# Kernel tuning notes

Measured on AMD Instinct MI355X. Metric: run time of the kernel, lower is better.

## Reference

```python
import jax, jax.numpy as jnp
import numpy as np

ALPHA = 0.1          # LeakyReLU negative slope
NEG = -9.0e15        # mask fill value (matches torch source)
S_OUT = 64           # source_out_features
T_OUT = 64           # target_out_features


def setup_inputs() -> dict:
    key = jax.random.key(0)
    ks = jax.random.split(key, 8)
    n_s, n_t = 8192, 4096
    s_in, t_in = 128, 128
    hs = jax.random.normal(ks[0], (n_s, s_in), dtype=jnp.float32)
    ht = jax.random.normal(ks[1], (n_t, t_in), dtype=jnp.float32)
    A_opt = jax.random.randint(ks[2], (n_t, n_s), 0, 2, dtype=jnp.int32)
    # xavier_uniform with gain=1.414
    def xavier(k, shape, gain=1.414):
        fan_in, fan_out = shape[0], shape[1]
        bound = gain * np.sqrt(6.0 / (fan_in + fan_out))
        return jax.random.uniform(k, shape, jnp.float32, -bound, bound)
    Ws = xavier(ks[3], (s_in, T_OUT))
    Wt = xavier(ks[4], (t_in, S_OUT))
    a1 = xavier(ks[5], (S_OUT + T_OUT, 1))
    bias_s = jnp.zeros((T_OUT,), jnp.float32)
    bias_t = jnp.zeros((S_OUT,), jnp.float32)
    return {"hs": hs, "ht": ht, "A_opt": A_opt, "Ws": Ws, "Wt": Wt,
            "a1": a1, "bias_s": bias_s, "bias_t": bias_t}


def reference(hs, ht, A_opt, Ws, Wt, a1, bias_s, bias_t):
    # Asymmetric HOAN, eval mode (dropout=0), concatenate=True.
    Whs = hs @ Ws                       # [n_s, t_out]
    Wht = ht @ Wt                       # [n_t, s_out]
    # a1 split: first S_OUT rows pair with Wht, remaining T_OUT rows with Whs
    a_t = a1[:S_OUT, :]                 # [s_out, 1]
    a_s = a1[S_OUT:, :]                 # [t_out, 1]
    Whst = Whs @ a_s                    # [n_s, 1]
    Whtt = Wht @ a_t                    # [n_t, 1]
    e_st = jax.nn.leaky_relu(Whtt + Whst.T, ALPHA)   # [n_t, n_s]
    e_ts = jax.nn.leaky_relu(Whst + Whtt.T, ALPHA)   # [n_s, n_t]
    mask = A_opt > 0                    # [n_t, n_s]
    att_st = jax.nn.softmax(jnp.where(mask, e_st, NEG), axis=1)
    h_prime_st = att_st @ Whs + bias_s  # [n_t, t_out]
    att_ts = jax.nn.softmax(jnp.where(mask.T, e_ts, NEG), axis=1)
    h_prime_ts = att_ts @ Wht + bias_t  # [n_s, s_out]
    return jax.nn.elu(h_prime_st), jax.nn.elu(h_prime_ts)
```

## Files before the change

kernel.cpp:

```cpp
#include <hip/hip_runtime.h>
#include <math.h>

#define N_S 8192
#define N_T 4096
#define DIN 128
#define NF  64
#define SPL0 8
#define SPL1 8

typedef __attribute__((ext_vector_type(8))) short short8;
typedef __attribute__((ext_vector_type(4))) float f32x4;
typedef unsigned long long u64;
typedef unsigned int u32;

__device__ __forceinline__ unsigned short f2bf(float x){
  unsigned u = __float_as_uint(x);
  unsigned r = (u + 0x7fffu + ((u >> 16) & 1u)) >> 16;
  return (unsigned short)r;
}

__device__ __forceinline__ size_t xt2_idx(int f, int k){
  return ((size_t)(k >> 5))*2048 + (size_t)((f >> 4)*512 + ((k >> 3) & 3)*128 + (f & 15)*8 + (k & 7));
}

__global__ __launch_bounds__(256) void k1_fused(
    const int* __restrict__ A,
    u64* __restrict__ RBt,
    u64* __restrict__ CBt,
    const float* __restrict__ hs, const float* __restrict__ ht,
    const float* __restrict__ Ws, const float* __restrict__ Wt,
    const float* __restrict__ a1,
    unsigned short* __restrict__ XT2s, unsigned short* __restrict__ XT2t,
    float* __restrict__ Es, float* __restrict__ Fs,
    float* __restrict__ Et, float* __restrict__ Ft)
{
  __shared__ __align__(16) float smem[DIN*NF + 4*DIN];
  int bx = blockIdx.x;
  int t = threadIdx.x;
  if (bx < 2048) {
    unsigned* T4 = (unsigned*)smem;
    int i0 = (bx & 63) * 64;
    int j0 = (bx >> 6) * 256;
    int w = t >> 6, l = t & 63;
    int4 v[16];
    #pragma unroll
    for (int it = 0; it < 16; ++it)
      v[it] = *(const int4*)&A[(size_t)(i0 + w*16 + it)*N_S + j0 + 4*l];
    #pragma unroll
    for (int rg = 0; rg < 4; ++rg) {
      unsigned p = 0;
      #pragma unroll
      for (int rr = 0; rr < 4; ++rr) {
        int4 m = v[rg*4 + rr];
        unsigned nib = (m.x > 0 ? 1u : 0u) | (m.y > 0 ? 2u : 0u)
                     | (m.z > 0 ? 4u : 0u) | (m.w > 0 ? 8u : 0u);
        p |= nib << (8*rr);
      }
      T4[(w*4 + rg)*65 + l] = p;
    }
    __syncthreads();
    {
      int r = t & 63, g = t >> 6;
      u64 bits = 0;
      #pragma unroll
      for (int i = 0; i < 16; ++i) {
        unsigned word = T4[(r >> 2)*65 + g*16 + i];
        unsigned nib = (word >> (8*(r & 3))) & 0xFu;
        bits |= (u64)nib << (4*i);
      }
      RBt[(size_t)((j0 >> 6) + g)*N_T + i0 + r] = bits;
    }
    {
      int c = t;
      u64 bits = 0;
      #pragma unroll
      for (int rg = 0; rg < 16; ++rg) {
        unsigned word = T4[rg*65 + (c >> 2)];
        unsigned x = (word >> (c & 3)) & 0x01010101u;
        unsigned nib = (x * 0x01020408u) >> 24;
        bits |= (u64)(nib & 0xFu) << (4*rg);
      }
      CBt[(size_t)(i0 >> 6)*N_S + j0 + c] = bits;
    }
  } else {
    int b = bx - 2048;
    float* Wl = smem;
    float* hrow = smem + DIN*NF;
    bool is_s = b < (N_S/4);
    const float* h; const float* W; const float* av;
    unsigned short* XT; float* Ed; float* Fd; int r0;
    if (is_s) { r0 = b*4;           h = hs; W = Ws; av = a1 + 64; XT = XT2s; Ed = Es; Fd = Fs; }
    else      { r0 = (b - N_S/4)*4; h = ht; W = Wt; av = a1;      XT = XT2t; Ed = Et; Fd = Ft; }
    for (int i = t; i < DIN*NF; i += 256) Wl[i] = W[i];
    for (int i = t; i < 4*DIN;  i += 256) hrow[i] = h[(size_t)r0*DIN + i];
    __syncthreads();
    int f = t & 63, sr = t >> 6;
    float acc = 0.f;
    #pragma unroll 8
    for (int k = 0; k < DIN; ++k) acc += hrow[sr*DIN + k] * Wl[k*NF + f];
    int r = r0 + sr;
    XT[xt2_idx(f, r)] = f2bf(acc);
    float p = acc * av[f];
    #pragma unroll
    for (int o = 32; o > 0; o >>= 1) p += __shfl_xor(p, o, 64);
    if (f == 0) { Ed[r] = __expf(p); Fd[r] = __expf(0.1f*p); }
  }
}

template<int DIR>
__device__ __forceinline__ void agg_body(
    int rb, int split,
    const u64* __restrict__ MBt,
    const float* __restrict__ EuT, const float* __restrict__ FuT,
    const float* __restrict__ EkT, const float* __restrict__ FkT,
    const unsigned short* __restrict__ XT2,
    float* __restrict__ accP,
    float* __restrict__ sumP)
{
  constexpr int NK = (DIR == 0) ? N_S : N_T;
  constexpr int NU = (DIR == 0) ? N_T : N_S;
  constexpr int SPL = (DIR == 0) ? SPL0 : SPL1;
  constexpr int KCH = NK / SPL;
  int t = threadIdx.x;
  int wave = t >> 6, l = t & 63;
  int row16 = l & 15, grp = l >> 4;
  int u = rb*64 + wave*16 + row16;
  float Eu = EuT[u], Fu = FuT[u];
  f32x4 acc[4];
  #pragma unroll
  for (int q = 0; q < 4; ++q) { acc[q][0]=0.f; acc[q][1]=0.f; acc[q][2]=0.f; acc[q][3]=0.f; }
  f32x4 accs; accs[0]=0.f; accs[1]=0.f; accs[2]=0.f; accs[3]=0.f;
  short8 bones;
  #pragma unroll
  for (int j = 0; j < 8; ++j) bones[j] = (short)0x3F80;
  int kc0 = split * KCH;

  #pragma unroll 2
  for (int k0 = kc0; k0 < kc0 + KCH; k0 += 64) {
    u64 mb = MBt[(size_t)(k0 >> 6)*NU + u];
    u32 mlo = (u32)mb, mhi = (u32)(mb >> 32);
    short8 af01[2];
    #pragma unroll
    for (int h = 0; h < 2; ++h) {
      int kb = k0 + 32*h + grp*8;
      float4 e0 = *(const float4*)&EkT[kb];
      float4 e1 = *(const float4*)&EkT[kb + 4];
      float4 f0 = *(const float4*)&FkT[kb];
      float4 f1 = *(const float4*)&FkT[kb + 4];
      float w0 = fmaxf(Eu*e0.x, Fu*f0.x);
      float w1 = fmaxf(Eu*e0.y, Fu*f0.y);
      float w2 = fmaxf(Eu*e0.z, Fu*f0.z);
      float w3 = fmaxf(Eu*e0.w, Fu*f0.w);
      float w4 = fmaxf(Eu*e1.x, Fu*f1.x);
      float w5 = fmaxf(Eu*e1.y, Fu*f1.y);
      float w6 = fmaxf(Eu*e1.z, Fu*f1.z);
      float w7 = fmaxf(Eu*e1.w, Fu*f1.w);
      u32 bb = ((h ? mhi : mlo) >> (grp*8)) & 0xffu;
      float wv[8] = {w0,w1,w2,w3,w4,w5,w6,w7};
      union { u32 uu[4]; short8 v; } pk;
      #pragma unroll
      for (int p = 0; p < 4; ++p) {
        int j = 2*p;
        int slo = ((int)(bb << (31 - j))) >> 31;
        int shi = ((int)(bb << (30 - j))) >> 31;
        u32 msk = __builtin_amdgcn_perm((u32)shi, (u32)slo, 0x05040100u);
        u32 w01 = __builtin_amdgcn_perm(__float_as_uint(wv[j+1]),
                                        __float_as_uint(wv[j]), 0x07060302u);
        pk.uu[p] = w01 & msk;
      }
      af01[h] = pk.v;
    }
    const unsigned short* xb = XT2 + ((size_t)(k0 >> 5))*2048 + l*8;
    #pragma unroll
    for (int q = 0; q < 4; ++q) {
      short8 b0 = *(const short8*)(xb + q*512);
      short8 b1 = *(const short8*)(xb + 2048 + q*512);
      acc[q] = __builtin_amdgcn_mfma_f32_16x16x32_bf16(af01[0], b0, acc[q], 0, 0, 0);
      acc[q] = __builtin_amdgcn_mfma_f32_16x16x32_bf16(af01[1], b1, acc[q], 0, 0, 0);
    }
    accs = __builtin_amdgcn_mfma_f32_16x16x32_bf16(af01[0], bones, accs, 0, 0, 0);
    accs = __builtin_amdgcn_mfma_f32_16x16x32_bf16(af01[1], bones, accs, 0, 0, 0);
  }

  if (row16 == 0) {
    #pragma unroll
    for (int r = 0; r < 4; ++r)
      sumP[(size_t)split*NU + rb*64 + wave*16 + grp*4 + r] = accs[r];
  }
  float* ap = accP + (size_t)split*NU*NF;
  #pragma unroll
  for (int q = 0; q < 4; ++q) {
    #pragma unroll
    for (int r = 0; r < 4; ++r) {
      int uo = rb*64 + wave*16 + grp*4 + r;
      ap[(size_t)uo*NF + q*16 + row16] = acc[q][r];
    }
  }
}

__global__ __launch_bounds__(256, 8) void agg_fused(
    const u64* __restrict__ RBt, const u64* __restrict__ CBt,
    const float* __restrict__ Es, const float* __restrict__ Fs,
    const float* __restrict__ Et, const float* __restrict__ Ft,
    const unsigned short* __restrict__ XT2s, const unsigned short* __restrict__ XT2t,
    float* __restrict__ P0, float* __restrict__ S0,
    float* __restrict__ P1, float* __restrict__ S1)
{
  int b = blockIdx.x;
  if (b < 64*SPL0) {
    agg_body<0>(b & 63, b >> 6, RBt, Et, Ft, Es, Fs, XT2s, P0, S0);
  } else {
    int b2 = b - 64*SPL0;
    agg_body<1>(b2 & 127, b2 >> 7, CBt, Es, Fs, Et, Ft, XT2t, P1, S1);
  }
}

__global__ __launch_bounds__(256) void finalize_kernel(
    const float* __restrict__ P0, const float* __restrict__ S0,
    const float* __restrict__ P1, const float* __restrict__ S1,
    const float* __restrict__ bias_s, const float* __restrict__ bias_t,
    float* __restrict__ out)
{
  int tid = blockIdx.x*256 + threadIdx.x;
  const int n0 = N_T*NF/4;
  float4 a = make_float4(0.f, 0.f, 0.f, 0.f);
  float den = 0.f;
  float4 bias;
  if (tid < n0) {
    int u = tid >> 4, fq = (tid & 15)*4;
    #pragma unroll
    for (int s = 0; s < SPL0; ++s) {
      float4 p = *(const float4*)&P0[((size_t)s*N_T + u)*NF + fq];
      a.x += p.x; a.y += p.y; a.z += p.z; a.w += p.w;
      den += S0[(size_t)s*N_T + u];
    }
    bias = *(const float4*)&bias_s[fq];
  } else {
    int i2 = tid - n0;
    int u = i2 >> 4, fq = (i2 & 15)*4;
    #pragma unroll
    for (int s = 0; s < SPL1; ++s) {
      float4 p = *(const float4*)&P1[((size_t)s*N_S + u)*NF + fq];
      a.x += p.x; a.y += p.y; a.z += p.z; a.w += p.w;
      den += S1[(size_t)s*N_S + u];
    }
    bias = *(const float4*)&bias_t[fq];
  }
  float inv = den > 0.f ? 1.f/den : 0.f;
  float4 v;
  v.x = a.x*inv + bias.x; v.y = a.y*inv + bias.y;
  v.z = a.z*inv + bias.z; v.w = a.w*inv + bias.w;
  v.x = v.x > 0.f ? v.x : expm1f(v.x);
  v.y = v.y > 0.f ? v.y : expm1f(v.y);
  v.z = v.z > 0.f ? v.z : expm1f(v.z);
  v.w = v.w > 0.f ? v.w : expm1f(v.w);
  *(float4*)&out[tid*4] = v;
}

extern "C" void kernel_launch(void* const* d_in, const int* in_sizes, int n_in,
                              void* d_out, int out_size, void* d_ws, size_t ws_size,
                              hipStream_t stream)
{
  const float* hs     = (const float*)d_in[0];
  const float* ht     = (const float*)d_in[1];
  const int*   A      = (const int*)  d_in[2];
  const float* Ws     = (const float*)d_in[3];
  const float* Wt     = (const float*)d_in[4];
  const float* a1     = (const float*)d_in[5];
  const float* bias_s = (const float*)d_in[6];
  const float* bias_t = (const float*)d_in[7];
  float* out = (float*)d_out;

  u64* RBt = (u64*)d_ws;
  u64* CBt = RBt + (size_t)(N_S/64)*N_T;
  unsigned short* XT2s = (unsigned short*)(CBt + (size_t)(N_T/64)*N_S);
  unsigned short* XT2t = XT2s + (size_t)NF*N_S;
  float* Es = (float*)(XT2t + (size_t)NF*N_T);
  float* Fs = Es + N_S;
  float* Et = Fs + N_S;
  float* Ft = Et + N_T;
  float* P0 = Ft + N_T;
  float* S0 = P0 + (size_t)SPL0*N_T*NF;
  float* P1 = S0 + (size_t)SPL0*N_T;
  float* S1 = P1 + (size_t)SPL1*N_S*NF;

  k1_fused<<<2048 + (N_S + N_T)/4, 256, 0, stream>>>(A, RBt, CBt, hs, ht, Ws, Wt, a1,
                                                     XT2s, XT2t, Es, Fs, Et, Ft);
  agg_fused<<<64*SPL0 + 128*SPL1, 256, 0, stream>>>(RBt, CBt, Es, Fs, Et, Ft,
                                                    XT2s, XT2t, P0, S0, P1, S1);
  finalize_kernel<<<(N_T*NF + N_S*NF)/1024, 256, 0, stream>>>(P0, S0, P1, S1,
                                                              bias_s, bias_t, out);
}
```

Before: 89.58 us.

## Interleave E/F arrays, chunk W staging, nontemporal mask loads, fewer splits

Stores the E and F exponentials for each node interleaved in one array, so the aggregation loop reads one stream of contiguous float4 pairs instead of two separate arrays. The projection blocks now stage W in 16-row chunks, cutting shared memory from about 33KB to about 6KB to raise occupancy, at the cost of extra barriers. The mask-packing loads of A use nontemporal hints to avoid polluting cache. The reverse-direction split count drops from 8 to 4, which means fewer partial sums to reduce but also fewer blocks in flight.

```diff
diff --git a/kernel.cpp b/kernel.cpp
--- a/kernel.cpp
+++ b/kernel.cpp
@@ -6,10 +6,11 @@
 #define DIN 128
 #define NF  64
 #define SPL0 8
-#define SPL1 8
+#define SPL1 4
 
 typedef __attribute__((ext_vector_type(8))) short short8;
 typedef __attribute__((ext_vector_type(4))) float f32x4;
+typedef __attribute__((ext_vector_type(4))) int i32x4;
 typedef unsigned long long u64;
 typedef unsigned int u32;
 
@@ -31,10 +32,9 @@
     const float* __restrict__ Ws, const float* __restrict__ Wt,
     const float* __restrict__ a1,
     unsigned short* __restrict__ XT2s, unsigned short* __restrict__ XT2t,
-    float* __restrict__ Es, float* __restrict__ Fs,
-    float* __restrict__ Et, float* __restrict__ Ft)
-{
-  __shared__ __align__(16) float smem[DIN*NF + 4*DIN];
+    float* __restrict__ EFs, float* __restrict__ EFt)
+{
+  __shared__ __align__(16) float smem[16*64 + 4*DIN];
   int bx = blockIdx.x;
   int t = threadIdx.x;
   if (bx < 2048) {
@@ -42,16 +42,17 @@
     int i0 = (bx & 63) * 64;
     int j0 = (bx >> 6) * 256;
     int w = t >> 6, l = t & 63;
-    int4 v[16];
+    i32x4 v[16];
     #pragma unroll
     for (int it = 0; it < 16; ++it)
-      v[it] = *(const int4*)&A[(size_t)(i0 + w*16 + it)*N_S + j0 + 4*l];
+      v[it] = __builtin_nontemporal_load(
+          (const i32x4*)&A[(size_t)(i0 + w*16 + it)*N_S + j0 + 4*l]);
     #pragma unroll
     for (int rg = 0; rg < 4; ++rg) {
       unsigned p = 0;
       #pragma unroll
       for (int rr = 0; rr < 4; ++rr) {
-        int4 m = v[rg*4 + rr];
+        i32x4 m = v[rg*4 + rr];
         unsigned nib = (m.x > 0 ? 1u : 0u) | (m.y > 0 ? 2u : 0u)
                      | (m.z > 0 ? 4u : 0u) | (m.w > 0 ? 8u : 0u);
         p |= nib << (8*rr);
@@ -85,25 +86,30 @@
   } else {
     int b = bx - 2048;
     float* Wl = smem;
-    float* hrow = smem + DIN*NF;
+    float* hrow = smem + 16*64;
     bool is_s = b < (N_S/4);
     const float* h; const float* W; const float* av;
-    unsigned short* XT; float* Ed; float* Fd; int r0;
-    if (is_s) { r0 = b*4;           h = hs; W = Ws; av = a1 + 64; XT = XT2s; Ed = Es; Fd = Fs; }
-    else      { r0 = (b - N_S/4)*4; h = ht; W = Wt; av = a1;      XT = XT2t; Ed = Et; Fd = Ft; }
-    for (int i = t; i < DIN*NF; i += 256) Wl[i] = W[i];
-    for (int i = t; i < 4*DIN;  i += 256) hrow[i] = h[(size_t)r0*DIN + i];
-    __syncthreads();
+    unsigned short* XT; float* EFd; int r0;
+    if (is_s) { r0 = b*4;           h = hs; W = Ws; av = a1 + 64; XT = XT2s; EFd = EFs; }
+    else      { r0 = (b - N_S/4)*4; h = ht; W = Wt; av = a1;      XT = XT2t; EFd = EFt; }
+    for (int i = t; i < 4*DIN; i += 256) hrow[i] = h[(size_t)r0*DIN + i];
     int f = t & 63, sr = t >> 6;
     float acc = 0.f;
-    #pragma unroll 8
-    for (int k = 0; k < DIN; ++k) acc += hrow[sr*DIN + k] * Wl[k*NF + f];
+    #pragma unroll
+    for (int c = 0; c < 8; ++c) {
+      __syncthreads();
+      #pragma unroll
+      for (int i = t; i < 16*64; i += 256) Wl[i] = W[(c*16 + (i >> 6))*NF + (i & 63)];
+      __syncthreads();
+      #pragma unroll
+      for (int kk = 0; kk < 16; ++kk) acc += hrow[sr*DIN + c*16 + kk] * Wl[kk*64 + f];
+    }
     int r = r0 + sr;
     XT[xt2_idx(f, r)] = f2bf(acc);
     float p = acc * av[f];
     #pragma unroll
     for (int o = 32; o > 0; o >>= 1) p += __shfl_xor(p, o, 64);
-    if (f == 0) { Ed[r] = __expf(p); Fd[r] = __expf(0.1f*p); }
+    if (f == 0) { EFd[2*r] = __expf(p); EFd[2*r + 1] = __expf(0.1f*p); }
   }
 }
 
@@ -111,8 +117,7 @@
 __device__ __forceinline__ void agg_body(
     int rb, int split,
     const u64* __restrict__ MBt,
-    const float* __restrict__ EuT, const float* __restrict__ FuT,
-    const float* __restrict__ EkT, const float* __restrict__ FkT,
+    const float* __restrict__ EFu, const float* __restrict__ EFk,
     const unsigned short* __restrict__ XT2,
     float* __restrict__ accP,
     float* __restrict__ sumP)
@@ -125,7 +130,8 @@
   int wave = t >> 6, l = t & 63;
   int row16 = l & 15, grp = l >> 4;
   int u = rb*64 + wave*16 + row16;
-  float Eu = EuT[u], Fu = FuT[u];
+  float2 ef = *(const float2*)&EFu[2*u];
+  float Eu = ef.x, Fu = ef.y;
   f32x4 acc[4];
   #pragma unroll
   for (int q = 0; q < 4; ++q) { acc[q][0]=0.f; acc[q][1]=0.f; acc[q][2]=0.f; acc[q][3]=0.f; }
@@ -143,20 +149,16 @@
     #pragma unroll
     for (int h = 0; h < 2; ++h) {
       int kb = k0 + 32*h + grp*8;
-      float4 e0 = *(const float4*)&EkT[kb];
-      float4 e1 = *(const float4*)&EkT[kb + 4];
-      float4 f0 = *(const float4*)&FkT[kb];
-      float4 f1 = *(const float4*)&FkT[kb + 4];
-      float w0 = fmaxf(Eu*e0.x, Fu*f0.x);
-      float w1 = fmaxf(Eu*e0.y, Fu*f0.y);
-      float w2 = fmaxf(Eu*e0.z, Fu*f0.z);
-      float w3 = fmaxf(Eu*e0.w, Fu*f0.w);
-      float w4 = fmaxf(Eu*e1.x, Fu*f1.x);
-      float w5 = fmaxf(Eu*e1.y, Fu*f1.y);
-      float w6 = fmaxf(Eu*e1.z, Fu*f1.z);
-      float w7 = fmaxf(Eu*e1.w, Fu*f1.w);
+      float4 p0 = *(const float4*)&EFk[2*kb];
+      float4 p1 = *(const float4*)&EFk[2*kb + 4];
+      float4 p2 = *(const float4*)&EFk[2*kb + 8];
+      float4 p3 = *(const float4*)&EFk[2*kb + 12];
+      float wv[8];
+      wv[0] = fmaxf(Eu*p0.x, Fu*p0.y); wv[1] = fmaxf(Eu*p0.z, Fu*p0.w);
+      wv[2] = fmaxf(Eu*p1.x, Fu*p1.y); wv[3] = fmaxf(Eu*p1.z, Fu*p1.w);
+      wv[4] = fmaxf(Eu*p2.x, Fu*p2.y); wv[5] = fmaxf(Eu*p2.z, Fu*p2.w);
+      wv[6] = fmaxf(Eu*p3.x, Fu*p3.y); wv[7] = fmaxf(Eu*p3.z, Fu*p3.w);
       u32 bb = ((h ? mhi : mlo) >> (grp*8)) & 0xffu;
-      float wv[8] = {w0,w1,w2,w3,w4,w5,w6,w7};
       union { u32 uu[4]; short8 v; } pk;
       #pragma unroll
       for (int p = 0; p < 4; ++p) {
@@ -200,18 +202,17 @@
 
 __global__ __launch_bounds__(256, 8) void agg_fused(
     const u64* __restrict__ RBt, const u64* __restrict__ CBt,
-    const float* __restrict__ Es, const float* __restrict__ Fs,
-    const float* __restrict__ Et, const float* __restrict__ Ft,
+    const float* __restrict__ EFs, const float* __restrict__ EFt,
     const unsigned short* __restrict__ XT2s, const unsigned short* __restrict__ XT2t,
     float* __restrict__ P0, float* __restrict__ S0,
     float* __restrict__ P1, float* __restrict__ S1)
 {
   int b = blockIdx.x;
   if (b < 64*SPL0) {
-    agg_body<0>(b & 63, b >> 6, RBt, Et, Ft, Es, Fs, XT2s, P0, S0);
+    agg_body<0>(b & 63, b >> 6, RBt, EFt, EFs, XT2s, P0, S0);
   } else {
     int b2 = b - 64*SPL0;
-    agg_body<1>(b2 & 127, b2 >> 7, CBt, Es, Fs, Et, Ft, XT2t, P1, S1);
+    agg_body<1>(b2 & 127, b2 >> 7, CBt, EFs, EFt, XT2t, P1, S1);
   }
 }
 
@@ -275,19 +276,17 @@
   u64* CBt = RBt + (size_t)(N_S/64)*N_T;
   unsigned short* XT2s = (unsigned short*)(CBt + (size_t)(N_T/64)*N_S);
   unsigned short* XT2t = XT2s + (size_t)NF*N_S;
-  float* Es = (float*)(XT2t + (size_t)NF*N_T);
-  float* Fs = Es + N_S;
-  float* Et = Fs + N_S;
-  float* Ft = Et + N_T;
-  float* P0 = Ft + N_T;
-  float* S0 = P0 + (size_t)SPL0*N_T*NF;
-  float* P1 = S0 + (size_t)SPL0*N_T;
-  float* S1 = P1 + (size_t)SPL1*N_S*NF;
+  float* EFs = (float*)(XT2t + (size_t)NF*N_T);
+  float* EFt = EFs + 2*N_S;
+  float* P0  = EFt + 2*N_T;
+  float* S0  = P0 + (size_t)SPL0*N_T*NF;
+  float* P1  = S0 + (size_t)SPL0*N_T;
+  float* S1  = P1 + (size_t)SPL1*N_S*NF;
 
   k1_fused<<<2048 + (N_S + N_T)/4, 256, 0, stream>>>(A, RBt, CBt, hs, ht, Ws, Wt, a1,
-                                                     XT2s, XT2t, Es, Fs, Et, Ft);
-  agg_fused<<<64*SPL0 + 128*SPL1, 256, 0, stream>>>(RBt, CBt, Es, Fs, Et, Ft,
-                                                    XT2s, XT2t, P0, S0, P1, S1);
+                                                     XT2s, XT2t, EFs, EFt);
+  agg_fused<<<64*SPL0 + 128*SPL1, 256, 0, stream>>>(RBt, CBt, EFs, EFt, XT2s, XT2t,
+                                                    P0, S0, P1, S1);
   finalize_kernel<<<(N_T*NF + N_S*NF)/1024, 256, 0, stream>>>(P0, S0, P1, S1,
                                                               bias_s, bias_t, out);
 }
```

Result: slower. 113.5 us (+26.7%).
